# Kernel optimization log

Hardware: AMD Instinct MI355X
Metric: run time of the kernel (lower is better)

Reference implementation:

```python
import jax, jax.numpy as jnp
import numpy as np

OUT_H = 7  # _height_
OUT_W = 7  # _width_


def _bin_ids(start, end, size, nbins):
    # Per-pixel segment id along one spatial axis; id == nbins marks pixels outside the ROI.
    # Mirrors TF: step = int(region / nbins); bin i covers [i*step, (i+1)*step), last bin extends to region end.
    step = ((end - start).astype(jnp.float32) / nbins).astype(jnp.int32)
    idx = jnp.arange(size)
    rel = idx - start
    b = jnp.minimum(rel // jnp.maximum(step, 1), nbins - 1)
    b = jnp.where(step > 0, b, nbins - 1)  # degenerate step==0: everything valid falls in last bin
    valid = (rel >= 0) & (idx < end)
    return jnp.where(valid, b, nbins)


def _pool_one(fmap, roi):
    # fmap: [H, W, C], roi: [4] = (h_min, w_min, h_max, w_max) relative coords
    H, W, C = fmap.shape
    h0 = (H * roi[0]).astype(jnp.int32)
    w0 = (W * roi[1]).astype(jnp.int32)
    h1 = (H * roi[2]).astype(jnp.int32)
    w1 = (W * roi[3]).astype(jnp.int32)
    colb = _bin_ids(w0, w1, W, OUT_W)  # [W]
    rowb = _bin_ids(h0, h1, H, OUT_H)  # [H]
    # Max is separable over rows/cols: pool columns first, then rows.
    tmp = jax.ops.segment_max(jnp.transpose(fmap, (1, 0, 2)), colb, num_segments=OUT_W + 1)[:OUT_W]  # [OUT_W, H, C]
    out = jax.ops.segment_max(jnp.transpose(tmp, (1, 0, 2)), rowb, num_segments=OUT_H + 1)[:OUT_H]   # [OUT_H, OUT_W, C]
    return out


def _roi_pool(feature_map, rois):
    per_image = jax.vmap(_pool_one, in_axes=(None, 0))  # over ROIs
    return jax.vmap(per_image)(feature_map, rois)       # over batch -> [B, R, OUT_H, OUT_W, C]


def setup_inputs() -> dict:
    key = jax.random.key(0)
    k1, k2, k3 = jax.random.split(key, 3)
    B, H, W, C, R = 4, 56, 56, 256, 64
    feature_map = jax.random.normal(k1, (B, H, W, C), dtype=jnp.float32)
    # valid ROIs: (h_min, w_min) in [0, 0.45), extent in [0.30, 0.55) so every 7x7 bin is non-empty
    starts = jax.random.uniform(k2, (B, R, 2), minval=0.0, maxval=0.45, dtype=jnp.float32)
    lens = jax.random.uniform(k3, (B, R, 2), minval=0.30, maxval=0.55, dtype=jnp.float32)
    rois = jnp.concatenate([starts, jnp.minimum(starts + lens, 1.0)], axis=-1)  # [B, R, 4]
    return {"feature_map": feature_map, "rois": rois}


def reference(feature_map, rois):
    return _roi_pool(feature_map, rois)
```

## Files before the change

kernel.cpp:

```cpp
#include <hip/hip_runtime.h>


#define OUT_H 7
#define OUT_W 7
#define NBIN (OUT_H * OUT_W)
#define NB 4
#define NR 64
#define NH 56
#define NW 56
#define NC 256
#define C4 (NC / 4)

#define NBLOCKS 1568
#define BLKS_PER_XCD_SLOT 196
#define BINS_PER_IMG (NR * NBIN)
#define PERM_MUL 597

typedef float v4f __attribute__((ext_vector_type(4)));

__device__ __forceinline__ v4f vmax4(v4f a, v4f b) {
    v4f r;
    r.x = fmaxf(a.x, b.x);
    r.y = fmaxf(a.y, b.y);
    r.z = fmaxf(a.z, b.z);
    r.w = fmaxf(a.w, b.w);
    return r;
}

__device__ __forceinline__ v4f pool_window(
    const v4f* __restrict__ base, int rlo, int rhi, int clo, int chi)
{
    const v4f ninf = (v4f){-INFINITY, -INFINITY, -INFINITY, -INFINITY};
    v4f acc0 = ninf, acc1 = ninf, acc2 = ninf, acc3 = ninf;

    int h = rlo;
    for (; h + 1 < rhi; h += 2) {
        const v4f* r0p = base + (size_t)(h * NW) * C4;
        const v4f* r1p = r0p + (size_t)NW * C4;
        int w = clo;
        for (; w + 1 < chi; w += 2) {
            acc0 = vmax4(acc0, r0p[(size_t)w * C4]);
            acc1 = vmax4(acc1, r0p[(size_t)(w + 1) * C4]);
            acc2 = vmax4(acc2, r1p[(size_t)w * C4]);
            acc3 = vmax4(acc3, r1p[(size_t)(w + 1) * C4]);
        }
        if (w < chi) {
            acc0 = vmax4(acc0, r0p[(size_t)w * C4]);
            acc2 = vmax4(acc2, r1p[(size_t)w * C4]);
        }
    }
    if (h < rhi) {
        const v4f* r0p = base + (size_t)(h * NW) * C4;
        int w = clo;
        for (; w + 1 < chi; w += 2) {
            acc0 = vmax4(acc0, r0p[(size_t)w * C4]);
            acc1 = vmax4(acc1, r0p[(size_t)(w + 1) * C4]);
        }
        if (w < chi) acc0 = vmax4(acc0, r0p[(size_t)w * C4]);
    }
    return vmax4(vmax4(acc0, acc1), vmax4(acc2, acc3));
}

__global__ __launch_bounds__(256, 8) void roi_pool_kernel(
    const float* __restrict__ fmap,
    const float* __restrict__ rois,
    float* __restrict__ out)
{
    const int blk  = blockIdx.x;
    const int xcd  = blk & 7;
    const int b    = xcd >> 1;
    const int wid  = threadIdx.x >> 6;
    const int lane = threadIdx.x & 63;

    const int ibl = ((xcd & 1) * BLKS_PER_XCD_SLOT) + (blk >> 3);
    const int iw  = ibl * 4 + wid;

    const v4f* base =
        (const v4f*)(fmap + (size_t)b * NH * NW * NC) + lane;
    const float* roib = rois + (size_t)b * NR * 4;

#pragma unroll
    for (int t = 0; t < 2; ++t) {
        const int j    = 2 * iw + t;
        const int gbin = (j * PERM_MUL) % BINS_PER_IMG;
        const int r    = gbin / NBIN;
        const int bin  = gbin - r * NBIN;
        const int oi   = bin / OUT_W;
        const int oj   = bin - oi * OUT_W;

        const float* roi = roib + (size_t)r * 4;
        const float r0 = roi[0], r1 = roi[1], r2 = roi[2], r3 = roi[3];
        const int h0 = (int)((float)NH * r0);
        const int w0 = (int)((float)NW * r1);
        const int h1 = (int)((float)NH * r2);
        const int w1 = (int)((float)NW * r3);

        const int hstep = (int)((float)(h1 - h0) / (float)OUT_H);
        const int wstep = (int)((float)(w1 - w0) / (float)OUT_W);

        int rlo, rhi, clo, chi;
        if (hstep >= 1) {
            rlo = h0 + oi * hstep;
            rhi = (oi < OUT_H - 1) ? (rlo + hstep) : h1;
        } else {
            rlo = (oi == OUT_H - 1) ? h0 : 0;
            rhi = (oi == OUT_H - 1) ? h1 : 0;
        }
        if (wstep >= 1) {
            clo = w0 + oj * wstep;
            chi = (oj < OUT_W - 1) ? (clo + wstep) : w1;
        } else {
            clo = (oj == OUT_W - 1) ? w0 : 0;
            chi = (oj == OUT_W - 1) ? w1 : 0;
        }

        const v4f m = pool_window(base, rlo, rhi, clo, chi);

        const size_t obase = ((size_t)((b * NR + r) * NBIN + bin)) * NC;
        v4f* o = (v4f*)(out + obase);
        __builtin_nontemporal_store(m, o + lane);
    }
}

extern "C" void kernel_launch(void* const* d_in, const int* in_sizes, int n_in,
                              void* d_out, int out_size, void* d_ws, size_t ws_size,
                              hipStream_t stream) {
    const float* fmap = (const float*)d_in[0];
    const float* rois = (const float*)d_in[1];
    float* out = (float*)d_out;

    roi_pool_kernel<<<NBLOCKS, 256, 0, stream>>>(fmap, rois, out);
}
```

Baseline: 16.27 us.

## Assign work by hardware XCD id via atomic rank counters and row strips

```diff
diff --git a/kernel.cpp b/kernel.cpp
--- a/kernel.cpp
+++ b/kernel.cpp
@@ -11,10 +11,8 @@
 #define NC 256
 #define C4 (NC / 4)
 
-#define NBLOCKS 1568
-#define BLKS_PER_XCD_SLOT 196
-#define BINS_PER_IMG (NR * NBIN)
-#define PERM_MUL 597
+#define RANKS_PER_XCD 224
+#define NBLOCKS 2048
 
 typedef float v4f __attribute__((ext_vector_type(4)));
 
@@ -64,48 +62,57 @@
 __global__ __launch_bounds__(256, 8) void roi_pool_kernel(
     const float* __restrict__ fmap,
     const float* __restrict__ rois,
-    float* __restrict__ out)
+    float* __restrict__ out,
+    int* __restrict__ cnt8)
 {
-    const int blk  = blockIdx.x;
-    const int xcd  = blk & 7;
-    const int b    = xcd >> 1;
+    __shared__ int s_rank;
+
+    unsigned xcc;
+    asm volatile("s_getreg_b32 %0, hwreg(20, 0, 32)" : "=s"(xcc));
+    const int x = (int)(xcc & 7u);
+
+    if (threadIdx.x == 0) s_rank = atomicAdd(&cnt8[x], 1);
+    __syncthreads();
+    const int rank = s_rank;
+    if (rank >= RANKS_PER_XCD) return;
+
+    const int b     = x >> 1;
+    const int strip = (x & 1) * RANKS_PER_XCD + rank;
+    const int r     = strip / OUT_H;
+    const int oi    = strip - r * OUT_H;
+
     const int wid  = threadIdx.x >> 6;
     const int lane = threadIdx.x & 63;
 
-    const int ibl = ((xcd & 1) * BLKS_PER_XCD_SLOT) + (blk >> 3);
-    const int iw  = ibl * 4 + wid;
+    const float* roi = rois + (size_t)(b * NR + r) * 4;
+    const float r0 = roi[0], r1 = roi[1], r2 = roi[2], r3 = roi[3];
+    const int h0 = (int)((float)NH * r0);
+    const int w0 = (int)((float)NW * r1);
+    const int h1 = (int)((float)NH * r2);
+    const int w1 = (int)((float)NW * r3);
+
+    const int hstep = (int)((float)(h1 - h0) / (float)OUT_H);
+    const int wstep = (int)((float)(w1 - w0) / (float)OUT_W);
+
+    int rlo, rhi;
+    if (hstep >= 1) {
+        rlo = h0 + oi * hstep;
+        rhi = (oi < OUT_H - 1) ? (rlo + hstep) : h1;
+    } else {
+        rlo = (oi == OUT_H - 1) ? h0 : 0;
+        rhi = (oi == OUT_H - 1) ? h1 : 0;
+    }
 
     const v4f* base =
         (const v4f*)(fmap + (size_t)b * NH * NW * NC) + lane;
-    const float* roib = rois + (size_t)b * NR * 4;
+    const size_t obase0 = ((size_t)((b * NR + r) * NBIN + oi * OUT_W)) * NC;
 
 #pragma unroll
     for (int t = 0; t < 2; ++t) {
-        const int j    = 2 * iw + t;
-        const int gbin = (j * PERM_MUL) % BINS_PER_IMG;
-        const int r    = gbin / NBIN;
-        const int bin  = gbin - r * NBIN;
-        const int oi   = bin / OUT_W;
-        const int oj   = bin - oi * OUT_W;
+        const int oj = wid + t * 4;
+        if (oj >= OUT_W) break;
 
-        const float* roi = roib + (size_t)r * 4;
-        const float r0 = roi[0], r1 = roi[1], r2 = roi[2], r3 = roi[3];
-        const int h0 = (int)((float)NH * r0);
-        const int w0 = (int)((float)NW * r1);
-        const int h1 = (int)((float)NH * r2);
-        const int w1 = (int)((float)NW * r3);
-
-        const int hstep = (int)((float)(h1 - h0) / (float)OUT_H);
-        const int wstep = (int)((float)(w1 - w0) / (float)OUT_W);
-
-        int rlo, rhi, clo, chi;
-        if (hstep >= 1) {
-            rlo = h0 + oi * hstep;
-            rhi = (oi < OUT_H - 1) ? (rlo + hstep) : h1;
-        } else {
-            rlo = (oi == OUT_H - 1) ? h0 : 0;
-            rhi = (oi == OUT_H - 1) ? h1 : 0;
-        }
+        int clo, chi;
         if (wstep >= 1) {
             clo = w0 + oj * wstep;
             chi = (oj < OUT_W - 1) ? (clo + wstep) : w1;
@@ -116,8 +123,7 @@
 
         const v4f m = pool_window(base, rlo, rhi, clo, chi);
 
-        const size_t obase = ((size_t)((b * NR + r) * NBIN + bin)) * NC;
-        v4f* o = (v4f*)(out + obase);
+        v4f* o = (v4f*)(out + obase0 + (size_t)oj * NC);
         __builtin_nontemporal_store(m, o + lane);
     }
 }
@@ -128,6 +134,9 @@
     const float* fmap = (const float*)d_in[0];
     const float* rois = (const float*)d_in[1];
     float* out = (float*)d_out;
+    int* cnt8 = (int*)d_ws;
 
-    roi_pool_kernel<<<NBLOCKS, 256, 0, stream>>>(fmap, rois, out);
+    hipMemsetAsync(cnt8, 0, 8 * sizeof(int), stream);
+
+    roi_pool_kernel<<<NBLOCKS, 256, 0, stream>>>(fmap, rois, out, cnt8);
 }
```

After: 43.06 us. +164.7%, slower.

## Precompute 2x2 max pyramid to cut per-bin window reads

Applied to the files above, without the earlier changes.

```diff
diff --git a/kernel.cpp b/kernel.cpp
--- a/kernel.cpp
+++ b/kernel.cpp
@@ -10,11 +10,17 @@
 #define NW 56
 #define NC 256
 #define C4 (NC / 4)
+#define NH2 (NH / 2)
+#define NW2 (NW / 2)
 
 #define NBLOCKS 1568
 #define BLKS_PER_XCD_SLOT 196
 #define BINS_PER_IMG (NR * NBIN)
 #define PERM_MUL 597
+
+#define P_ELEMS ((size_t)NB * NH2 * NW * NC)
+#define Q_ELEMS ((size_t)NB * NH2 * NW2 * NC)
+#define WS_NEEDED (((size_t)P_ELEMS + Q_ELEMS) * sizeof(float))
 
 typedef float v4f __attribute__((ext_vector_type(4)));
 
@@ -27,12 +33,38 @@
     return r;
 }
 
-__device__ __forceinline__ v4f pool_window(
+__global__ __launch_bounds__(64) void build_pyr(
+    const float* __restrict__ fmap, float* __restrict__ P, float* __restrict__ Q)
+{
+    const int blk   = blockIdx.x;
+    const int b     = blk / 112;
+    const int rem   = blk - b * 112;
+    const int h2    = rem >> 2;
+    const int chunk = rem & 3;
+    const int c0    = chunk * 14;
+    const int lane  = threadIdx.x;
+
+    const v4f* F0 = (const v4f*)(fmap + ((size_t)(b * NH + 2 * h2) * NW) * NC) + lane;
+    const v4f* F1 = F0 + (size_t)NW * C4;
+    v4f* Pp = (v4f*)(P + ((size_t)(b * NH2 + h2) * NW) * NC) + lane;
+    v4f* Qp = (v4f*)(Q + ((size_t)(b * NH2 + h2) * NW2) * NC) + lane;
+
+    v4f pprev;
+#pragma unroll
+    for (int k = 0; k < 14; ++k) {
+        const int w = c0 + k;
+        v4f p = vmax4(F0[(size_t)w * C4], F1[(size_t)w * C4]);
+        Pp[(size_t)w * C4] = p;
+        if (k & 1) Qp[(size_t)(w >> 1) * C4] = vmax4(pprev, p);
+        pprev = p;
+    }
+}
+
+__device__ __forceinline__ v4f pool_window_direct(
     const v4f* __restrict__ base, int rlo, int rhi, int clo, int chi)
 {
     const v4f ninf = (v4f){-INFINITY, -INFINITY, -INFINITY, -INFINITY};
     v4f acc0 = ninf, acc1 = ninf, acc2 = ninf, acc3 = ninf;
-
     int h = rlo;
     for (; h + 1 < rhi; h += 2) {
         const v4f* r0p = base + (size_t)(h * NW) * C4;
@@ -61,10 +93,56 @@
     return vmax4(vmax4(acc0, acc1), vmax4(acc2, acc3));
 }
 
+__device__ __forceinline__ v4f pool_window_pyr(
+    const v4f* __restrict__ Fb, const v4f* __restrict__ Pb,
+    const v4f* __restrict__ Qb, int rlo, int rhi, int clo, int chi)
+{
+    const v4f ninf = (v4f){-INFINITY, -INFINITY, -INFINITY, -INFINITY};
+    if (rhi <= rlo || chi <= clo) return ninf;
+
+    const int p_lo = (rlo + 1) >> 1, p_hi = rhi >> 1;
+    const int er0  = (rlo & 1) ? rlo : -1;
+    const int er1  = (rhi & 1) ? (rhi - 1) : -1;
+    const int q_lo = (clo + 1) >> 1, q_hi = chi >> 1;
+    const int ec0  = (clo & 1) ? clo : -1;
+    const int ec1  = (chi & 1) ? (chi - 1) : -1;
+
+    v4f a0 = ninf, a1 = ninf;
+
+    for (int p = p_lo; p < p_hi; ++p) {
+        const v4f* Qrow = Qb + (size_t)(p * NW2) * C4;
+        const v4f* Prow = Pb + (size_t)(p * NW) * C4;
+        int q = q_lo;
+        for (; q + 1 < q_hi; q += 2) {
+            a0 = vmax4(a0, Qrow[(size_t)q * C4]);
+            a1 = vmax4(a1, Qrow[(size_t)(q + 1) * C4]);
+        }
+        if (q < q_hi) a0 = vmax4(a0, Qrow[(size_t)q * C4]);
+        if (ec0 >= 0) a0 = vmax4(a0, Prow[(size_t)ec0 * C4]);
+        if (ec1 >= 0) a1 = vmax4(a1, Prow[(size_t)ec1 * C4]);
+    }
+#pragma unroll
+    for (int e = 0; e < 2; ++e) {
+        const int er = e ? er1 : er0;
+        if (er < 0) continue;
+        const v4f* Frow = Fb + (size_t)(er * NW) * C4;
+        int w = clo;
+        for (; w + 1 < chi; w += 2) {
+            a0 = vmax4(a0, Frow[(size_t)w * C4]);
+            a1 = vmax4(a1, Frow[(size_t)(w + 1) * C4]);
+        }
+        if (w < chi) a0 = vmax4(a0, Frow[(size_t)w * C4]);
+    }
+    return vmax4(a0, a1);
+}
+
+template <bool USE_PYR>
 __global__ __launch_bounds__(256, 8) void roi_pool_kernel(
     const float* __restrict__ fmap,
     const float* __restrict__ rois,
-    float* __restrict__ out)
+    float* __restrict__ out,
+    const float* __restrict__ P,
+    const float* __restrict__ Q)
 {
     const int blk  = blockIdx.x;
     const int xcd  = blk & 7;
@@ -75,8 +153,9 @@
     const int ibl = ((xcd & 1) * BLKS_PER_XCD_SLOT) + (blk >> 3);
     const int iw  = ibl * 4 + wid;
 
-    const v4f* base =
-        (const v4f*)(fmap + (size_t)b * NH * NW * NC) + lane;
+    const v4f* Fb = (const v4f*)(fmap + (size_t)b * NH * NW * NC) + lane;
+    const v4f* Pb = (const v4f*)(P + (size_t)b * NH2 * NW * NC) + lane;
+    const v4f* Qb = (const v4f*)(Q + (size_t)b * NH2 * NW2 * NC) + lane;
     const float* roib = rois + (size_t)b * NR * 4;
 
 #pragma unroll
@@ -114,7 +193,11 @@
             chi = (oj == OUT_W - 1) ? w1 : 0;
         }
 
-        const v4f m = pool_window(base, rlo, rhi, clo, chi);
+        v4f m;
+        if (USE_PYR)
+            m = pool_window_pyr(Fb, Pb, Qb, rlo, rhi, clo, chi);
+        else
+            m = pool_window_direct(Fb, rlo, rhi, clo, chi);
 
         const size_t obase = ((size_t)((b * NR + r) * NBIN + bin)) * NC;
         v4f* o = (v4f*)(out + obase);
@@ -129,5 +212,13 @@
     const float* rois = (const float*)d_in[1];
     float* out = (float*)d_out;
 
-    roi_pool_kernel<<<NBLOCKS, 256, 0, stream>>>(fmap, rois, out);
-}
+    if (ws_size >= WS_NEEDED) {
+        float* P = (float*)d_ws;
+        float* Q = P + P_ELEMS;
+        build_pyr<<<NB * NH2 * 4, 64, 0, stream>>>(fmap, P, Q);
+        roi_pool_kernel<true><<<NBLOCKS, 256, 0, stream>>>(fmap, rois, out, P, Q);
+    } else {
+        roi_pool_kernel<false><<<NBLOCKS, 256, 0, stream>>>(fmap, rois, out,
+                                                            nullptr, nullptr);
+    }
+}
```

Result: slower. 21.89 us (+34.6%).
